# Kernel optimization log

Measured on AMD Instinct MI355X. Metric: run time of the kernel, lower is better.

## Reference

```python
import jax, jax.numpy as jnp
import numpy as np
from jax import lax

N, T, H, W, E = 512, 10, 40, 40, 8192

def _conv2d(x, w, b):
    y = lax.conv_general_dilated(x, w, (1, 1), 'SAME',
                                 dimension_numbers=('NCHW', 'OIHW', 'NCHW'))
    return y + b[None, :, None, None]

def _bn_per_t(x, g, b, eps=1e-5):
    # x: (N, T, C, H, W); torch training-mode BN stats computed per timestep (loop over t in original)
    mu = x.mean(axis=(0, 3, 4), keepdims=True)
    var = x.var(axis=(0, 3, 4), keepdims=True)
    return g[None, None, :, None, None] * (x - mu) * lax.rsqrt(var + eps) + b[None, None, :, None, None]

def _maxpool2(x):
    return lax.reduce_window(x, -jnp.inf, lax.max, (1, 1, 2, 2), (1, 1, 2, 2), 'VALID')

def _cnn(x, w1, b1, g1, be1, w2, b2, g2, be2):
    # conv3x3 -> BN -> relu -> maxpool2 -> conv3x3 -> BN -> relu -> adaptive avgpool(5,5); x: (N,T,Cin,H,W)
    n, t, c, h, w = x.shape
    y = _conv2d(x.reshape(n * t, c, h, w), w1, b1).reshape(n, t, 16, h, w)
    y = jax.nn.relu(_bn_per_t(y, g1, be1))
    y = _maxpool2(y.reshape(n * t, 16, h, w))
    y = _conv2d(y, w2, b2)
    co = w2.shape[0]
    y = jax.nn.relu(_bn_per_t(y.reshape(n, t, co, h // 2, w // 2), g2, be2))
    k = (h // 2) // 5  # 20 -> 5 is a uniform 4x4 average pool
    y = y.reshape(n, t, co, 5, k, 5, k).mean(axis=(4, 6))
    return y.reshape(n, t, co * 25)

def _sage(x, src, dst, wl, bl, wr):
    # PyG SAGEConv(aggr='max'): lin_l(max-aggregated neighbor feats) + lin_r(x); x: (T,N,F)
    t, n, f = x.shape
    msgs = x[:, src]                                               # (T,E,F) gather
    agg = jnp.full((t, n, f), -jnp.inf, x.dtype).at[:, dst].max(msgs)
    agg = jnp.where(jnp.isfinite(agg), agg, 0.0)                   # isolated nodes -> 0 (PyG convention)
    return jnp.einsum('tnf,of->tno', agg, wl) + bl + jnp.einsum('tnf,of->tno', x, wr)

def _lstm_last(x, wih, whh, bih, bhh):
    # x: (T,N,F); torch gate order i,f,g,o; returns final hidden state h_T
    t, n, _ = x.shape
    hdim = whh.shape[1]
    def step(carry, xt):
        h, c = carry
        z = xt @ wih.T + bih + h @ whh.T + bhh
        i, f, g, o = jnp.split(z, 4, axis=-1)
        c = jax.nn.sigmoid(f) * c + jax.nn.sigmoid(i) * jnp.tanh(g)
        h = jax.nn.sigmoid(o) * jnp.tanh(c)
        return (h, c), None
    init = (jnp.zeros((n, hdim), x.dtype), jnp.zeros((n, hdim), x.dtype))
    (h, _), _ = lax.scan(step, init, x)
    return h

def _forward(veg, cwsi, irrigation, edge_index, vw1, vb1, vg1, vbe1, vw2, vb2, vg2, vbe2,
             cw1, cb1, cg1, cbe1, cw2, cb2, cg2, cbe2, emb,
             s1_wl, s1_bl, s1_wr, s2_wl, s2_bl, s2_wr, wih, whh, bih, bhh, fcw, fcb):
    vfeat = _cnn(veg, vw1, vb1, vg1, vbe1, vw2, vb2, vg2, vbe2)    # (N,T,400)
    cfeat = _cnn(cwsi, cw1, cb1, cg1, cbe1, cw2, cb2, cg2, cbe2)   # (N,T,200)
    ifeat = emb[irrigation]                                        # (N,T,16)
    feats = jnp.concatenate([vfeat, cfeat, ifeat], axis=-1).transpose(1, 0, 2)  # (T,N,616)
    src, dst = edge_index[0], edge_index[1]
    x = jax.nn.relu(_sage(feats, src, dst, s1_wl, s1_bl, s1_wr))
    x = jax.nn.relu(_sage(x, src, dst, s2_wl, s2_bl, s2_wr))       # (T,N,32)
    h = _lstm_last(x, wih, whh, bih, bhh)                          # (N,64)
    return h @ fcw.T + fcb                                         # (N,1)

def setup_inputs():
    key = jax.random.key(0)
    ks = jax.random.split(key, 16)
    w = lambda i, shape: jax.random.normal(ks[i], shape, jnp.float32) * 0.05
    return dict(
        veg=jax.random.normal(ks[0], (N, T, 5, H, W), jnp.float32),
        cwsi=jax.random.normal(ks[1], (N, T, 1, H, W), jnp.float32),
        irrigation=jax.random.randint(ks[2], (N, T), 0, 3, jnp.int32),
        edge_index=jax.random.randint(ks[3], (2, E), 0, N, jnp.int32),
        vw1=w(4, (16, 5, 3, 3)), vb1=jnp.zeros(16), vg1=jnp.ones(16), vbe1=jnp.zeros(16),
        vw2=w(5, (16, 16, 3, 3)), vb2=jnp.zeros(16), vg2=jnp.ones(16), vbe2=jnp.zeros(16),
        cw1=w(6, (16, 1, 3, 3)), cb1=jnp.zeros(16), cg1=jnp.ones(16), cbe1=jnp.zeros(16),
        cw2=w(7, (8, 16, 3, 3)), cb2=jnp.zeros(8), cg2=jnp.ones(8), cbe2=jnp.zeros(8),
        emb=jax.random.normal(ks[8], (3, 16), jnp.float32),
        s1_wl=w(9, (64, 616)), s1_bl=jnp.zeros(64), s1_wr=w(10, (64, 616)),
        s2_wl=w(11, (32, 64)), s2_bl=jnp.zeros(32), s2_wr=w(12, (32, 64)),
        wih=w(13, (256, 32)), whh=w(14, (256, 64)), bih=jnp.zeros(256), bhh=jnp.zeros(256),
        fcw=w(15, (1, 64)), fcb=jnp.zeros(1),
    )

def reference(veg, cwsi, irrigation, edge_index, vw1, vb1, vg1, vbe1, vw2, vb2, vg2, vbe2,
              cw1, cb1, cg1, cbe1, cw2, cb2, cg2, cbe2, emb,
              s1_wl, s1_bl, s1_wr, s2_wl, s2_bl, s2_wr, wih, whh, bih, bhh, fcw, fcb):
    return _forward(veg, cwsi, irrigation, edge_index, vw1, vb1, vg1, vbe1, vw2, vb2, vg2, vbe2,
                    cw1, cb1, cg1, cbe1, cw2, cb2, cg2, cbe2, emb,
                    s1_wl, s1_bl, s1_wr, s2_wl, s2_bl, s2_wr, wih, whh, bih, bhh, fcw, fcb)
```

## Files before the change

kernel.cpp:

```cpp
#include <hip/hip_runtime.h>
#include <math.h>

#define NBATCH 512
#define TSTEPS 10
#define NIMG   5120
#define FEAT   616
#define NEDGE  8192

__device__ __forceinline__ float sigf(float x){ return 1.f/(1.f + expf(-x)); }

__global__ void prep_kernel(const float* __restrict__ s1wl, const float* __restrict__ s1wr,
                            const float* __restrict__ s2wl, const float* __restrict__ s2wr,
                            const float* __restrict__ wih,  const float* __restrict__ whh,
                            float* __restrict__ wlT, float* __restrict__ wrT,
                            float* __restrict__ wl2T, float* __restrict__ wr2T,
                            float* __restrict__ wihT, float* __restrict__ whhT,
                            double* __restrict__ stats)
{
  int idx = blockIdx.x*256 + threadIdx.x;
  if (idx < 39424){ wlT[(idx%616)*64 + idx/616] = s1wl[idx]; return; }
  idx -= 39424;
  if (idx < 39424){ wrT[(idx%616)*64 + idx/616] = s1wr[idx]; return; }
  idx -= 39424;
  if (idx < 2048){ wl2T[(idx%64)*32 + idx/64] = s2wl[idx]; return; }
  idx -= 2048;
  if (idx < 2048){ wr2T[(idx%64)*32 + idx/64] = s2wr[idx]; return; }
  idx -= 2048;
  if (idx < 8192){ wihT[(idx%32)*256 + idx/32] = wih[idx]; return; }
  idx -= 8192;
  if (idx < 16384){ whhT[(idx%64)*256 + idx/64] = whh[idx]; return; }
  idx -= 16384;
  if (idx < 1280){ stats[idx] = 0.0; }
}

__global__ void csr_kernel(const int* __restrict__ edges, int* __restrict__ row_start,
                           int* __restrict__ adj)
{
  __shared__ int cnt_s[512];
  __shared__ int scan_s[512];
  const int tid = threadIdx.x;
  const int* src = edges;
  const int* dst = edges + NEDGE;
  cnt_s[tid] = 0;
  __syncthreads();
  for (int e = tid; e < NEDGE; e += 512) atomicAdd(&cnt_s[dst[e]], 1);
  __syncthreads();
  int v = cnt_s[tid];
  scan_s[tid] = v;
  __syncthreads();
  for (int off = 1; off < 512; off <<= 1){
    int add = (tid >= off) ? scan_s[tid - off] : 0;
    __syncthreads();
    scan_s[tid] += add;
    __syncthreads();
  }
  int start = scan_s[tid] - v;
  row_start[tid] = start;
  if (tid == 511) row_start[512] = scan_s[511];
  cnt_s[tid] = start;
  __syncthreads();
  for (int e = tid; e < NEDGE; e += 512){
    int d = dst[e];
    int pos = atomicAdd(&cnt_s[d], 1);
    adj[pos] = src[e];
  }
}

template<int CIN>
__launch_bounds__(320, 4)
__global__ void conv1_kernel(const float* __restrict__ in, const float* __restrict__ w,
                             double* __restrict__ stats, float* __restrict__ premax)
{
  __shared__ __attribute__((aligned(16))) float in_t[CIN*792];
  __shared__ __attribute__((aligned(16))) float wl[CIN*144];
  __shared__ __attribute__((aligned(16))) float red[2560];
  const int tid = threadIdx.x;
  const int bid = blockIdx.x;
  const int img = bid / 3, strip = bid % 3;
  const int y0 = strip * 16;
  const int t = img % TSTEPS;
  const float* imgp = in + (size_t)img * CIN * 1600;

  for (int idx = tid; idx < CIN*144; idx += 320){
    int co = idx & 15, rest = idx >> 4;
    int k = rest % 9, ci = rest / 9;
    wl[(ci*9 + k)*16 + co] = w[(co*CIN + ci)*9 + k];
  }
  {
    const int r0 = tid / 44, c0 = tid % 44;
    #pragma unroll
    for (int ci = 0; ci < CIN; ci++){
      const float* ip = imgp + ci*1600;
      float* ot = &in_t[ci*792];
      int r = r0, c = c0;
      #pragma unroll
      for (int k = 0; k < 3; k++){
        int idx = tid + k*320;
        if (idx < 792){
          int gy = y0 + r - 1, gx = c - 1;
          float v = 0.f;
          if ((unsigned)gy < 40u && (unsigned)gx < 40u) v = ip[gy*40 + gx];
          ot[r*44 + c] = v;
        }
        r += 7; c += 12; if (c >= 44){ c -= 44; r += 1; }
      }
    }
  }
  __syncthreads();

  const int pos = tid % 80, cog = tid / 80;
  const int row = pos & 15, oct = pos >> 4;
  const int x8 = oct * 8;
  const int co0 = cog * 4;
  const int gy = y0 + row;
  const bool act = gy < 40;

  float acc[8][4];
  #pragma unroll
  for (int i = 0; i < 8; i++)
    #pragma unroll
    for (int j = 0; j < 4; j++) acc[i][j] = 0.f;

  for (int ci = 0; ci < CIN; ci++){
    float v[3][10];
    #pragma unroll
    for (int r = 0; r < 3; r++){
      const float* rp = &in_t[ci*792 + (row + r)*44 + x8];
      const float4 a = *(const float4*)rp;
      const float4 b = *(const float4*)(rp + 4);
      const float2 c = *(const float2*)(rp + 8);
      v[r][0] = a.x; v[r][1] = a.y; v[r][2] = a.z; v[r][3] = a.w;
      v[r][4] = b.x; v[r][5] = b.y; v[r][6] = b.z; v[r][7] = b.w;
      v[r][8] = c.x; v[r][9] = c.y;
    }
    #pragma unroll
    for (int dy = 0; dy < 3; dy++)
      #pragma unroll
      for (int dx = 0; dx < 3; dx++){
        const float4 wv = *(const float4*)&wl[(ci*9 + dy*3 + dx)*16 + co0];
        #pragma unroll
        for (int px = 0; px < 8; px++){
          float iv = v[dy][px + dx];
          acc[px][0] += iv*wv.x; acc[px][1] += iv*wv.y;
          acc[px][2] += iv*wv.z; acc[px][3] += iv*wv.w;
        }
      }
  }

  #pragma unroll
  for (int cl = 0; cl < 4; cl++){
    float s = 0.f, q = 0.f;
    #pragma unroll
    for (int px = 0; px < 8; px++){
      float a = acc[px][cl];
      s += a; q += a*a;
    }
    red[(co0 + cl)*80 + pos]        = act ? s : 0.f;
    red[1280 + (co0 + cl)*80 + pos] = act ? q : 0.f;
  }

  {
    const int py = strip*8 + (row >> 1);
    #pragma unroll
    for (int cl = 0; cl < 4; cl++){
      float hp[4];
      #pragma unroll
      for (int j = 0; j < 4; j++)
        hp[j] = fmaxf(acc[2*j][cl], acc[2*j + 1][cl]);
      float op[4];
      #pragma unroll
      for (int j = 0; j < 4; j++) op[j] = __shfl_xor(hp[j], 1, 64);
      if (act && !(row & 1)){
        float4 r4;
        r4.x = fmaxf(hp[0], op[0]); r4.y = fmaxf(hp[1], op[1]);
        r4.z = fmaxf(hp[2], op[2]); r4.w = fmaxf(hp[3], op[3]);
        *(float4*)&premax[(size_t)img*6400 + (co0 + cl)*400 + py*20 + oct*4] = r4;
      }
    }
  }

  __syncthreads();
  if (tid < 256){
    int co = tid >> 4, seg = tid & 15;
    float vs = 0.f, vq = 0.f;
    #pragma unroll
    for (int j = 0; j < 5; j++){
      vs += red[co*80 + seg*5 + j];
      vq += red[1280 + co*80 + seg*5 + j];
    }
    #pragma unroll
    for (int off = 8; off > 0; off >>= 1){
      vs += __shfl_down(vs, off, 16);
      vq += __shfl_down(vq, off, 16);
    }
    if (seg == 0){
      atomicAdd(&stats[(t*16 + co)*2 + 0], (double)vs);
      atomicAdd(&stats[(t*16 + co)*2 + 1], (double)vq);
    }
  }
}

template<int CO>
__launch_bounds__(256, 4)
__global__ void conv2_kernel(float* __restrict__ pooled, const float* __restrict__ w,
                             const float* __restrict__ bnp1, double* __restrict__ stats)
{
  constexpr int R = (CO == 16) ? 2 : 1;
  constexpr int P = (20/R) * 5;
  __shared__ __attribute__((aligned(16))) float in_t[16*528];
  __shared__ __attribute__((aligned(16))) float wl[144*CO];
  const int tid = threadIdx.x;
  const int img = blockIdx.x;
  const int t = img % TSTEPS;
  const size_t ib = (size_t)img * 6400;

  for (int idx = tid; idx < 144*CO; idx += 256){
    int co = idx % CO, rest = idx / CO;
    int k = rest % 9, ci = rest / 9;
    wl[(ci*9 + k)*CO + co] = w[(co*16 + ci)*9 + k];
  }
  {
    const int r0 = tid / 24, c0 = tid % 24;
    for (int ci = 0; ci < 16; ci++){
      const float sc = bnp1[(t*16 + ci)*2 + 0];
      const float sh = bnp1[(t*16 + ci)*2 + 1];
      const float* ip = pooled + ib + ci*400;
      float* ot = &in_t[ci*528];
      int r = r0, c = c0;
      #pragma unroll
      for (int k = 0; k < 3; k++){
        int idx = tid + k*256;
        if (idx < 528){
          int gy = r - 1, gx = c - 1;
          float v = 0.f;
          if ((unsigned)gy < 20u && (unsigned)gx < 20u)
            v = fmaxf(sc*ip[gy*20 + gx] + sh, 0.f);
          ot[r*24 + c] = v;
        }
        r += 10; c += 16; if (c >= 24){ c -= 24; r += 1; }
      }
    }
  }
  __syncthreads();

  const bool act = tid < P*(CO/4);
  const int q = tid % P, cog = tid / P;
  const int x4 = (q % 5) * 4, yb = (q / 5) * R;
  const int co0 = cog * 4;
  float acc[R][4][4];
  #pragma unroll
  for (int rr = 0; rr < R; rr++)
    #pragma unroll
    for (int i = 0; i < 4; i++)
      #pragma unroll
      for (int j = 0; j < 4; j++) acc[rr][i][j] = 0.f;

  if (act){
    for (int ci = 0; ci < 16; ci++){
      float v[R + 2][6];
      #pragma unroll
      for (int r = 0; r < R + 2; r++){
        const float* rp = &in_t[ci*528 + (yb + r)*24 + x4];
        const float4 a = *(const float4*)rp;
        const float2 b = *(const float2*)(rp + 4);
        v[r][0] = a.x; v[r][1] = a.y; v[r][2] = a.z; v[r][3] = a.w;
        v[r][4] = b.x; v[r][5] = b.y;
      }
      #pragma unroll
      for (int dy = 0; dy < 3; dy++)
        #pragma unroll
        for (int dx = 0; dx < 3; dx++){
          const float4 wv = *(const float4*)&wl[(ci*9 + dy*3 + dx)*CO + co0];
          #pragma unroll
          for (int rr = 0; rr < R; rr++){
            #pragma unroll
            for (int px = 0; px < 4; px++){
              float iv = v[rr + dy][px + dx];
              acc[rr][px][0] += iv*wv.x; acc[rr][px][1] += iv*wv.y;
              acc[rr][px][2] += iv*wv.z; acc[rr][px][3] += iv*wv.w;
            }
          }
        }
    }
    #pragma unroll
    for (int cl = 0; cl < 4; cl++)
      #pragma unroll
      for (int rr = 0; rr < R; rr++){
        float4 o4;
        o4.x = acc[rr][0][cl]; o4.y = acc[rr][1][cl];
        o4.z = acc[rr][2][cl]; o4.w = acc[rr][3][cl];
        *(float4*)&pooled[ib + (co0 + cl)*400 + (yb + rr)*20 + x4] = o4;
      }
  }
  __syncthreads();

  if (act){
    #pragma unroll
    for (int cl = 0; cl < 4; cl++){
      float s = 0.f, qq = 0.f;
      #pragma unroll
      for (int rr = 0; rr < R; rr++)
        #pragma unroll
        for (int px = 0; px < 4; px++){
          float a = acc[rr][px][cl];
          s += a; qq += a*a;
        }
      in_t[(co0 + cl)*P + q]            = s;
      in_t[CO*P + (co0 + cl)*P + q]     = qq;
    }
  }
  __syncthreads();
  if (tid < CO*8){
    int co = tid >> 3, seg = tid & 7;
    float vs = 0.f, vq = 0.f;
    for (int j = seg; j < P; j += 8){
      vs += in_t[co*P + j];
      vq += in_t[CO*P + co*P + j];
    }
    #pragma unroll
    for (int off = 4; off > 0; off >>= 1){
      vs += __shfl_down(vs, off, 8);
      vq += __shfl_down(vq, off, 8);
    }
    if (seg == 0){
      atomicAdd(&stats[(t*CO + co)*2 + 0], (double)vs);
      atomicAdd(&stats[(t*CO + co)*2 + 1], (double)vq);
    }
  }
}

template<int CO>
__global__ void bnavg_kernel(const float* __restrict__ raw, const float* __restrict__ bnp,
                             float* __restrict__ feats, int featBase)
{
  const int img = blockIdx.x;
  const int t = img % TSTEPS, n = img / TSTEPS;
  for (int idx = threadIdx.x; idx < CO*25; idx += 256){
    int co = idx / 25, q = idx % 25, py = q / 5, px = q % 5;
    float sc = bnp[(t*CO + co)*2 + 0];
    float sh = bnp[(t*CO + co)*2 + 1];
    const float* base = raw + (size_t)img*6400 + co*400 + (py*4)*20 + px*4;
    float s = 0.f;
    #pragma unroll
    for (int r = 0; r < 4; r++){
      float4 v = *(const float4*)(base + r*20);
      s += fmaxf(v.x*sc + sh, 0.f) + fmaxf(v.y*sc + sh, 0.f)
         + fmaxf(v.z*sc + sh, 0.f) + fmaxf(v.w*sc + sh, 0.f);
    }
    feats[(size_t)(t*NBATCH + n)*FEAT + featBase + idx] = s * 0.0625f;
  }
}

__global__ void bn_param_kernel(const double* __restrict__ stats, float* __restrict__ bnp,
                                const float* __restrict__ g, const float* __restrict__ be,
                                int C, double invCnt)
{
  int idx = threadIdx.x;
  if (idx < TSTEPS*C){
    int c = idx % C;
    double mean = stats[idx*2] * invCnt;
    double var  = stats[idx*2 + 1] * invCnt - mean*mean;
    if (var < 0.0) var = 0.0;
    double sc = (double)g[c] / sqrt(var + 1e-5);
    bnp[idx*2]     = (float)sc;
    bnp[idx*2 + 1] = be[c] - (float)(mean * sc);
  }
}

__global__ void emb_kernel(const int* __restrict__ irr, const float* __restrict__ emb,
                           float* __restrict__ feats)
{
  int idx = blockIdx.x*256 + threadIdx.x;
  if (idx >= NBATCH*TSTEPS*16) return;
  int k = idx & 15;
  int nt = idx >> 4;
  int t = nt % TSTEPS, n = nt / TSTEPS;
  feats[(size_t)(t*NBATCH + n)*FEAT + 600 + k] = emb[irr[nt]*16 + k];
}

__global__ void agg_kernel(const float* __restrict__ feats, const int* __restrict__ row_start,
                           const int* __restrict__ adj, float* __restrict__ agg)
{
  __shared__ int adjs[192];
  const int bid = blockIdx.x;
  const int t = bid / NBATCH, n = bid % NBATCH;
  const int tid = threadIdx.x;
  const int rs = row_start[n], re = row_start[n + 1];
  const int deg = re - rs;
  for (int i = tid; i < deg && i < 192; i += 256) adjs[i] = adj[rs + i];
  __syncthreads();
  const float* fb = feats + (size_t)t*NBATCH*FEAT;
  float* ab = agg + (size_t)(t*NBATCH + n)*FEAT;
  for (int f = tid; f < FEAT; f += 256){
    float m = -1e30f;
    for (int j = 0; j < deg; j++){
      int s = (j < 192) ? adjs[j] : adj[rs + j];
      m = fmaxf(m, fb[(size_t)s*FEAT + f]);
    }
    ab[f] = (deg > 0) ? m : 0.f;
  }
}

__launch_bounds__(256)
__global__ void sage1_kernel(const float* __restrict__ feats, const float* __restrict__ agg,
                             const float* __restrict__ wlT, const float* __restrict__ wrT,
                             const float* __restrict__ bl, float* __restrict__ x1)
{
  __shared__ float xr[4][616];
  __shared__ float ar[4][616];
  const int tid = threadIdx.x;
  const int bid = blockIdx.x;
  for (int idx = tid; idx < 4*616; idx += 256){
    int r = idx / 616, f = idx % 616;
    size_t row = (size_t)bid*4 + r;
    xr[r][f] = feats[row*FEAT + f];
    ar[r][f] = agg[row*FEAT + f];
  }
  __syncthreads();
  const int wid = tid >> 6, o = tid & 63;
  const int row = bid*4 + wid;
  float acc = bl[o];
  #pragma unroll 4
  for (int f = 0; f < 616; f++){
    acc += ar[wid][f]*wlT[f*64 + o] + xr[wid][f]*wrT[f*64 + o];
  }
  x1[(size_t)row*64 + o] = fmaxf(acc, 0.f);
}

__launch_bounds__(64)
__global__ void sage2_kernel(const float* __restrict__ x1, const int* __restrict__ row_start,
                             const int* __restrict__ adj, const float* __restrict__ wl2T,
                             const float* __restrict__ wr2T, const float* __restrict__ bl2,
                             float* __restrict__ x2)
{
  __shared__ float am[64], xm[64];
  __shared__ int adjs[192];
  const int bid = blockIdx.x;
  const int t = bid / NBATCH, n = bid % NBATCH;
  const int lane = threadIdx.x;
  const int rs = row_start[n], re = row_start[n + 1];
  const int deg = re - rs;
  for (int i = lane; i < deg && i < 192; i += 64) adjs[i] = adj[rs + i];
  __syncthreads();
  const float* xb = x1 + (size_t)t*NBATCH*64;
  float m = -1e30f;
  for (int j = 0; j < deg; j++){
    int s = (j < 192) ? adjs[j] : adj[rs + j];
    m = fmaxf(m, xb[s*64 + lane]);
  }
  am[lane] = (deg > 0) ? m : 0.f;
  xm[lane] = xb[n*64 + lane];
  __syncthreads();
  if (lane < 32){
    float acc = bl2[lane];
    #pragma unroll 4
    for (int f = 0; f < 64; f++){
      acc += am[f]*wl2T[f*32 + lane] + xm[f]*wr2T[f*32 + lane];
    }
    x2[(size_t)(t*NBATCH + n)*32 + lane] = fmaxf(acc, 0.f);
  }
}

__launch_bounds__(256)
__global__ void lstm_kernel(const float* __restrict__ x2, const float* __restrict__ wihT,
                            const float* __restrict__ whhT, const float* __restrict__ bih,
                            const float* __restrict__ bhh, const float* __restrict__ fcw,
                            const float* __restrict__ fcb, float* __restrict__ out)
{
  __shared__ float xb[32], hb[64], cbuf[64], zb[256];
  const int n = blockIdx.x;
  const int tid = threadIdx.x;
  if (tid < 64){ hb[tid] = 0.f; cbuf[tid] = 0.f; }
  __syncthreads();
  const float bsum = bih[tid] + bhh[tid];
  for (int t = 0; t < TSTEPS; t++){
    if (tid < 32) xb[tid] = x2[(size_t)(t*NBATCH + n)*32 + tid];
    __syncthreads();
    float acc = bsum;
    #pragma unroll 8
    for (int k = 0; k < 32; k++) acc += xb[k]*wihT[k*256 + tid];
    #pragma unroll 8
    for (int k = 0; k < 64; k++) acc += hb[k]*whhT[k*256 + tid];
    zb[tid] = acc;
    __syncthreads();
    if (tid < 64){
      float zi = zb[tid], zf = zb[64 + tid], zg = zb[128 + tid], zo = zb[192 + tid];
      float c = sigf(zf)*cbuf[tid] + sigf(zi)*tanhf(zg);
      cbuf[tid] = c;
      hb[tid] = sigf(zo)*tanhf(c);
    }
    __syncthreads();
  }
  if (tid < 64){
    float v = hb[tid]*fcw[tid];
    #pragma unroll
    for (int off = 32; off > 0; off >>= 1) v += __shfl_down(v, off, 64);
    if (tid == 0) out[n] = v + fcb[0];
  }
}

extern "C" void kernel_launch(void* const* d_in, const int* in_sizes, int n_in,
                              void* d_out, int out_size, void* d_ws, size_t ws_size,
                              hipStream_t stream)
{
  const float* veg  = (const float*)d_in[0];
  const float* cwsi = (const float*)d_in[1];
  const int*   irr  = (const int*)d_in[2];
  const int*   eidx = (const int*)d_in[3];
  const float* vw1  = (const float*)d_in[4];
  const float* vg1  = (const float*)d_in[6];
  const float* vbe1 = (const float*)d_in[7];
  const float* vw2  = (const float*)d_in[8];
  const float* vg2  = (const float*)d_in[10];
  const float* vbe2 = (const float*)d_in[11];
  const float* cw1  = (const float*)d_in[12];
  const float* cg1  = (const float*)d_in[14];
  const float* cbe1 = (const float*)d_in[15];
  const float* cw2  = (const float*)d_in[16];
  const float* cg2  = (const float*)d_in[18];
  const float* cbe2 = (const float*)d_in[19];
  const float* emb  = (const float*)d_in[20];
  const float* s1wl = (const float*)d_in[21];
  const float* s1bl = (const float*)d_in[22];
  const float* s1wr = (const float*)d_in[23];
  const float* s2wl = (const float*)d_in[24];
  const float* s2bl = (const float*)d_in[25];
  const float* s2wr = (const float*)d_in[26];
  const float* wih  = (const float*)d_in[27];
  const float* whh  = (const float*)d_in[28];
  const float* bih  = (const float*)d_in[29];
  const float* bhh  = (const float*)d_in[30];
  const float* fcw  = (const float*)d_in[31];
  const float* fcb  = (const float*)d_in[32];
  float* out = (float*)d_out;

  float* ws = (float*)d_ws;
  size_t off = 0;
  float* pooled = ws + off; off += (size_t)NIMG*6400;
  float* feats  = ws + off; off += (size_t)NIMG*FEAT;
  float* agg1   = ws + off; off += (size_t)NIMG*FEAT;
  float* x1     = ws + off; off += (size_t)NIMG*64;
  float* x2     = ws + off; off += (size_t)NIMG*32;
  float* wlT    = ws + off; off += 39424;
  float* wrT    = ws + off; off += 39424;
  float* wl2T   = ws + off; off += 2048;
  float* wr2T   = ws + off; off += 2048;
  float* wihT   = ws + off; off += 8192;
  float* whhT   = ws + off; off += 16384;
  off = (off + 1) & ~(size_t)1;
  double* stats = (double*)(ws + off); off += 2560;
  float* bnp    = ws + off; off += 1280;
  int* row_start= (int*)(ws + off); off += 513;
  int* adj      = (int*)(ws + off); off += 8192;
  (void)in_sizes; (void)n_in; (void)out_size; (void)ws_size;

  prep_kernel<<<425, 256, 0, stream>>>(s1wl, s1wr, s2wl, s2wr, wih, whh,
                                       wlT, wrT, wl2T, wr2T, wihT, whhT, stats);
  csr_kernel<<<1, 512, 0, stream>>>(eidx, row_start, adj);

  double* stV1 = stats;        float* bnV1 = bnp;
  double* stV2 = stats + 320;  float* bnV2 = bnp + 320;
  double* stC1 = stats + 640;  float* bnC1 = bnp + 640;
  double* stC2 = stats + 960;  float* bnC2 = bnp + 960;

  conv1_kernel<5><<<NIMG*3, 320, 0, stream>>>(veg, vw1, stV1, pooled);
  bn_param_kernel<<<1, 256, 0, stream>>>(stV1, bnV1, vg1, vbe1, 16, 1.0/(512.0*1600.0));
  conv2_kernel<16><<<NIMG, 256, 0, stream>>>(pooled, vw2, bnV1, stV2);
  bn_param_kernel<<<1, 256, 0, stream>>>(stV2, bnV2, vg2, vbe2, 16, 1.0/(512.0*400.0));
  bnavg_kernel<16><<<NIMG, 256, 0, stream>>>(pooled, bnV2, feats, 0);

  conv1_kernel<1><<<NIMG*3, 320, 0, stream>>>(cwsi, cw1, stC1, pooled);
  bn_param_kernel<<<1, 256, 0, stream>>>(stC1, bnC1, cg1, cbe1, 16, 1.0/(512.0*1600.0));
  conv2_kernel<8><<<NIMG, 256, 0, stream>>>(pooled, cw2, bnC1, stC2);
  bn_param_kernel<<<1, 256, 0, stream>>>(stC2, bnC2, cg2, cbe2, 8, 1.0/(512.0*400.0));
  bnavg_kernel<8><<<NIMG, 256, 0, stream>>>(pooled, bnC2, feats, 400);

  emb_kernel<<<(NBATCH*TSTEPS*16 + 255)/256, 256, 0, stream>>>(irr, emb, feats);
  agg_kernel<<<NIMG, 256, 0, stream>>>(feats, row_start, adj, agg1);
  sage1_kernel<<<NIMG/4, 256, 0, stream>>>(feats, agg1, wlT, wrT, s1bl, x1);
  sage2_kernel<<<NIMG, 64, 0, stream>>>(x1, row_start, adj, wl2T, wr2T, s2bl, x2);
  lstm_kernel<<<NBATCH, 256, 0, stream>>>(x2, wihT, whhT, bih, bhh, fcw, fcb, out);
}
```

Baseline: 879.0 us.

## Interleave channel groups across lanes and reduce BN stats with wave shuffles

Changes the thread-to-work mapping in conv1 and conv2 so the output-channel group varies fastest across lanes. Threads in a wave then share spatial positions and read the same input tile rows from shared memory, while the per-thread weight reads differ. In conv1 the BN sum and sum-of-squares reduction now uses cross-lane xor shuffles followed by a small shared buffer, replacing the 10KB shared reduction array. The maxpool partner shuffle is adjusted to match the new layout. The occupancy hints are also dropped from both launch bounds, which may let the compiler use more registers at the cost of fewer resident waves.

Result: slower. 1.060 ms (+20.6%).

```diff
diff --git a/kernel.cpp b/kernel.cpp
--- a/kernel.cpp
+++ b/kernel.cpp
@@ -67,13 +67,13 @@
 }
 
 template<int CIN>
-__launch_bounds__(320, 4)
+__launch_bounds__(320)
 __global__ void conv1_kernel(const float* __restrict__ in, const float* __restrict__ w,
                              double* __restrict__ stats, float* __restrict__ premax)
 {
   __shared__ __attribute__((aligned(16))) float in_t[CIN*792];
   __shared__ __attribute__((aligned(16))) float wl[CIN*144];
-  __shared__ __attribute__((aligned(16))) float red[2560];
+  __shared__ __attribute__((aligned(16))) float red2[160];
   const int tid = threadIdx.x;
   const int bid = blockIdx.x;
   const int img = bid / 3, strip = bid % 3;
@@ -108,7 +108,7 @@
   }
   __syncthreads();
 
-  const int pos = tid % 80, cog = tid / 80;
+  const int cog = tid & 3, pos = tid >> 2;
   const int row = pos & 15, oct = pos >> 4;
   const int x8 = oct * 8;
   const int co0 = cog * 4;
@@ -147,16 +147,35 @@
       }
   }
 
-  #pragma unroll
-  for (int cl = 0; cl < 4; cl++){
-    float s = 0.f, q = 0.f;
-    #pragma unroll
-    for (int px = 0; px < 8; px++){
-      float a = acc[px][cl];
-      s += a; q += a*a;
-    }
-    red[(co0 + cl)*80 + pos]        = act ? s : 0.f;
-    red[1280 + (co0 + cl)*80 + pos] = act ? q : 0.f;
+  {
+    float s4[4], q4[4];
+    #pragma unroll
+    for (int cl = 0; cl < 4; cl++){
+      float s = 0.f, q = 0.f;
+      #pragma unroll
+      for (int px = 0; px < 8; px++){
+        float a = acc[px][cl];
+        s += a; q += a*a;
+      }
+      s4[cl] = act ? s : 0.f;
+      q4[cl] = act ? q : 0.f;
+    }
+    #pragma unroll
+    for (int off = 4; off <= 32; off <<= 1){
+      #pragma unroll
+      for (int cl = 0; cl < 4; cl++){
+        s4[cl] += __shfl_xor(s4[cl], off, 64);
+        q4[cl] += __shfl_xor(q4[cl], off, 64);
+      }
+    }
+    const int lane = tid & 63, wid = tid >> 6;
+    if (lane < 4){
+      #pragma unroll
+      for (int cl = 0; cl < 4; cl++){
+        red2[((wid*4 + lane)*4 + cl)*2 + 0] = s4[cl];
+        red2[((wid*4 + lane)*4 + cl)*2 + 1] = q4[cl];
+      }
+    }
   }
 
   {
@@ -169,7 +188,7 @@
         hp[j] = fmaxf(acc[2*j][cl], acc[2*j + 1][cl]);
       float op[4];
       #pragma unroll
-      for (int j = 0; j < 4; j++) op[j] = __shfl_xor(hp[j], 1, 64);
+      for (int j = 0; j < 4; j++) op[j] = __shfl_xor(hp[j], 4, 64);
       if (act && !(row & 1)){
         float4 r4;
         r4.x = fmaxf(hp[0], op[0]); r4.y = fmaxf(hp[1], op[1]);
@@ -180,33 +199,27 @@
   }
 
   __syncthreads();
-  if (tid < 256){
-    int co = tid >> 4, seg = tid & 15;
+  if (tid < 16){
+    const int cg = tid >> 2, cl = tid & 3;
     float vs = 0.f, vq = 0.f;
     #pragma unroll
-    for (int j = 0; j < 5; j++){
-      vs += red[co*80 + seg*5 + j];
-      vq += red[1280 + co*80 + seg*5 + j];
-    }
-    #pragma unroll
-    for (int off = 8; off > 0; off >>= 1){
-      vs += __shfl_down(vs, off, 16);
-      vq += __shfl_down(vq, off, 16);
-    }
-    if (seg == 0){
-      atomicAdd(&stats[(t*16 + co)*2 + 0], (double)vs);
-      atomicAdd(&stats[(t*16 + co)*2 + 1], (double)vq);
-    }
+    for (int wd = 0; wd < 5; wd++){
+      vs += red2[((wd*4 + cg)*4 + cl)*2 + 0];
+      vq += red2[((wd*4 + cg)*4 + cl)*2 + 1];
+    }
+    atomicAdd(&stats[(t*16 + tid)*2 + 0], (double)vs);
+    atomicAdd(&stats[(t*16 + tid)*2 + 1], (double)vq);
   }
 }
 
 template<int CO>
-__launch_bounds__(256, 4)
+__launch_bounds__(256)
 __global__ void conv2_kernel(float* __restrict__ pooled, const float* __restrict__ w,
                              const float* __restrict__ bnp1, double* __restrict__ stats)
 {
   constexpr int R = (CO == 16) ? 2 : 1;
   constexpr int P = (20/R) * 5;
+  constexpr int G = CO/4;
   __shared__ __attribute__((aligned(16))) float in_t[16*528];
   __shared__ __attribute__((aligned(16))) float wl[144*CO];
   const int tid = threadIdx.x;
@@ -243,8 +256,8 @@
   }
   __syncthreads();
 
-  const bool act = tid < P*(CO/4);
-  const int q = tid % P, cog = tid / P;
+  const int cog = tid & (G - 1), q = tid / G;
+  const bool act = q < P;
   const int x4 = (q % 5) * 4, yb = (q / 5) * R;
   const int co0 = cog * 4;
   float acc[R][4][4];
```
